# Performance work log

Measured on AMD Instinct MI355X. Metric: run time of the kernel, lower is better.

The kernel has to match this reference:

```python
import jax, jax.numpy as jnp
import numpy as np

N_NODES = 100000
N_EDGES = 1600000
N_GRAPHS = 1024
B = 1024
GNN_INP, GNN_HID, GNN_OUT = 64, 128, 64
INP, HID, OUT = 64, 256, 1
EPS = 1e-5  # torch BatchNorm1d default eps


def _bn(h, gamma, beta):
    # training-mode BatchNorm1d: biased batch statistics over dim 0
    m = h.mean(axis=0)
    v = jnp.mean((h - m) ** 2, axis=0)
    return (h - m) * jax.lax.rsqrt(v + EPS) * gamma + beta


def setup_inputs() -> dict:
    key = jax.random.key(0)
    ks = jax.random.split(key, 24)
    s = 0.05
    inp = {
        "x": jax.random.normal(ks[0], (B, INP), jnp.float32),
        "masks": jax.random.randint(ks[1], (B,), 0, N_GRAPHS),
        "gnn_x": jax.random.normal(ks[2], (N_NODES, GNN_INP), jnp.float32),
        "edge_index": jax.random.randint(ks[3], (2, N_EDGES), 0, N_NODES),
        "gnn_batch": jnp.sort(jax.random.randint(ks[4], (N_NODES,), 0, N_GRAPHS)),
        # GCNConv params
        "W_gcn": jax.random.normal(ks[5], (GNN_INP, GNN_HID), jnp.float32) * s,
        "b_gcn": jnp.zeros((GNN_HID,), jnp.float32),
        "g1": jnp.ones((GNN_HID,), jnp.float32), "be1": jnp.zeros((GNN_HID,), jnp.float32),
        "W_lin1": jax.random.normal(ks[6], (GNN_HID, GNN_HID // 2), jnp.float32) * s,
        "b_lin1": jnp.zeros((GNN_HID // 2,), jnp.float32),
        "g2": jnp.ones((GNN_HID // 2,), jnp.float32), "be2": jnp.zeros((GNN_HID // 2,), jnp.float32),
        "W_lin2": jax.random.normal(ks[7], (GNN_HID // 2, GNN_OUT), jnp.float32) * s,
        "b_lin2": jnp.zeros((GNN_OUT,), jnp.float32),
        "g3": jnp.ones((GNN_OUT,), jnp.float32), "be3": jnp.zeros((GNN_OUT,), jnp.float32),
        # head params
        "W_fc1": jax.random.normal(ks[8], (INP + GNN_OUT, HID), jnp.float32) * s,
        "b_fc1": jnp.zeros((HID,), jnp.float32),
        "g4": jnp.ones((HID,), jnp.float32), "be4": jnp.zeros((HID,), jnp.float32),
        "W_fc2": jax.random.normal(ks[9], (HID, HID // 4), jnp.float32) * s,
        "b_fc2": jnp.zeros((HID // 4,), jnp.float32),
        "g5": jnp.ones((HID // 4,), jnp.float32), "be5": jnp.zeros((HID // 4,), jnp.float32),
        "W_fc3": jax.random.normal(ks[10], (HID // 4, OUT), jnp.float32) * s,
        "b_fc3": jnp.zeros((OUT,), jnp.float32),
    }
    return inp


def _forward(x, masks, gnn_x, edge_index, gnn_batch,
             W_gcn, b_gcn, g1, be1, W_lin1, b_lin1, g2, be2, W_lin2, b_lin2,
             g3, be3, W_fc1, b_fc1, g4, be4, W_fc2, b_fc2, g5, be5, W_fc3, b_fc3):
    N = gnn_x.shape[0]
    # --- GCNConv: linear transform, self-loops, sym-normalized scatter-add ---
    h = gnn_x @ W_gcn  # [N, GNN_HID]
    loop = jnp.arange(N)
    src = jnp.concatenate([edge_index[0], loop])
    dst = jnp.concatenate([edge_index[1], loop])
    deg = jax.ops.segment_sum(jnp.ones_like(dst, jnp.float32), dst, num_segments=N)
    dis = jax.lax.rsqrt(deg)  # deg >= 1 thanks to self-loops
    norm = dis[src] * dis[dst]  # [E+N]
    agg = jax.ops.segment_sum(h[src] * norm[:, None], dst, num_segments=N) + b_gcn
    z = jax.nn.relu(_bn(agg, g1, be1))  # dropout = identity (eval)
    # --- global_mean_pool over graph ids ---
    sums = jax.ops.segment_sum(z, gnn_batch, num_segments=N_GRAPHS)
    cnt = jax.ops.segment_sum(jnp.ones((N,), jnp.float32), gnn_batch, num_segments=N_GRAPHS)
    pooled = sums / jnp.maximum(cnt, 1.0)[:, None]  # [G, GNN_HID]
    z = jax.nn.relu(_bn(pooled @ W_lin1 + b_lin1, g2, be2))
    z = _bn(z @ W_lin2 + b_lin2, g3, be3)  # [G, GNN_OUT]
    # --- MixGNN head ---
    g = z[masks]  # [B, GNN_OUT]
    t = jnp.concatenate([x, g], axis=1)
    t = jax.nn.relu(_bn(t @ W_fc1 + b_fc1, g4, be4))
    t = t * t  # Multiply([h, h])
    t = jax.nn.relu(_bn(t @ W_fc2 + b_fc2, g5, be5))
    t = t * t
    t = t * t
    return t @ W_fc3 + b_fc3  # [B, OUT]


def reference(x, masks, gnn_x, edge_index, gnn_batch,
              W_gcn, b_gcn, g1, be1, W_lin1, b_lin1, g2, be2, W_lin2, b_lin2,
              g3, be3, W_fc1, b_fc1, g4, be4, W_fc2, b_fc2, g5, be5, W_fc3, b_fc3):
    return _forward(x, masks, gnn_x, edge_index, gnn_batch,
                    W_gcn, b_gcn, g1, be1, W_lin1, b_lin1, g2, be2, W_lin2, b_lin2,
                    g3, be3, W_fc1, b_fc1, g4, be4, W_fc2, b_fc2, g5, be5, W_fc3, b_fc3)
```

## Files before the change

### kernel.cpp

```cpp
#include <hip/hip_runtime.h>
#include <hip/hip_bf16.h>

#define N_NODES 100000
#define N_EDGES 1600000
#define N_GRAPHS 1024
#define BSZ 1024
#define EPS 1e-5f

#define NBUCK 256
#define BUCKW 391
#define BCAP  8192
#define SRC_MASK 0x1FFFF
#define BIN_CHUNK 4096
#define BIN_BLOCKS 391
#define NCHUNK 512
#define CHUNK_ROWS 196

#define WS_PSUM    0
#define WS_STATS1  131072
#define WS_STATS2  131200
#define WS_STATS4  131328
#define WS_STATS5  131840
#define WS_M       131968
#define WS_CS      136064
#define WS_ZTOTAL  136128
#define WS_GCUR    136128
#define WS_SCALE1  136384
#define WS_SHIFTP  136512
#define WS_GSTART  136640
#define WS_DIS     137668
#define WS_ROWPTR  237668
#define WS_ROWLEN  337668
#define WS_PACKED  437668
#define WS_CSRC    2534820
#define WS_XH      4631972
#define WS_AGGX    7831972
#define WS_T1      14231972
#define WS_T2      14297508
#define WS_T4      14363044
#define WS_T5      14625188

__device__ inline unsigned short f2bf(float f) {
    unsigned int u = __float_as_uint(f);
    return (unsigned short)((u + 0x7FFFu + ((u >> 16) & 1u)) >> 16);
}

__global__ __launch_bounds__(256) void prep_kernel(float* __restrict__ ws,
                                                   const int* __restrict__ gbatch) {
    int b = blockIdx.x, tid = threadIdx.x;
    if (b < 16) {
        for (int i = b * 256 + tid; i < WS_ZTOTAL; i += 16 * 256) ws[i] = 0.0f;
    } else if (b == 16) {
        ((int*)(ws + WS_GCUR))[tid] = tid * BCAP;
    } else {
        int g = (b - 17) * 256 + tid;
        int lo = 0, hi = N_NODES;
        while (lo < hi) {
            int mid = (lo + hi) >> 1;
            if (gbatch[mid] < g) lo = mid + 1; else hi = mid;
        }
        int* gstart = (int*)(ws + WS_GSTART);
        gstart[g] = lo;
        if (g == 0) gstart[N_GRAPHS] = N_NODES;
    }
}

__global__ __launch_bounds__(256) void cvt_kernel(const float* __restrict__ x,
                                                  unsigned short* __restrict__ xh) {
    int i = blockIdx.x * 256 + threadIdx.x;
    float4 f = ((const float4*)x)[i];
    ushort4 h;
    h.x = f2bf(f.x); h.y = f2bf(f.y); h.z = f2bf(f.z); h.w = f2bf(f.w);
    ((ushort4*)xh)[i] = h;
}

__global__ __launch_bounds__(512) void bin_kernel(const int* __restrict__ ei,
                                                  int* __restrict__ gcursor,
                                                  unsigned int* __restrict__ packed) {
    __shared__ unsigned int stage[BIN_CHUNK];
    __shared__ int lh[NBUCK], lbase[NBUCK], lcur[NBUCK], gb[NBUCK];
    const int* src = ei;
    const int* dst = ei + N_EDGES;
    int tid = threadIdx.x;
    int base = blockIdx.x * BIN_CHUNK;
    int n = min(BIN_CHUNK, N_EDGES - base);
    if (tid < NBUCK) lh[tid] = 0;
    __syncthreads();
    for (int i = tid; i < n; i += 512)
        atomicAdd(&lh[dst[base + i] / BUCKW], 1);
    __syncthreads();
    if (tid < NBUCK) lbase[tid] = lh[tid];
    __syncthreads();
    for (int off = 1; off < NBUCK; off <<= 1) {
        int t = (tid < NBUCK && tid >= off) ? lbase[tid - off] : 0;
        __syncthreads();
        if (tid < NBUCK) lbase[tid] += t;
        __syncthreads();
    }
    if (tid < NBUCK) {
        int excl = lbase[tid] - lh[tid];
        lbase[tid] = excl;
        lcur[tid] = excl;
        gb[tid] = atomicAdd(&gcursor[tid], lh[tid]);
    }
    __syncthreads();
    for (int i = tid; i < n; i += 512) {
        int d = dst[base + i];
        int s = src[base + i];
        int bk = d / BUCKW;
        int dl = d - bk * BUCKW;
        int slot = atomicAdd(&lcur[bk], 1);
        stage[slot] = ((unsigned int)dl << 17) | (unsigned int)s;
    }
    __syncthreads();
    int wid = tid >> 6, lane = tid & 63;
    for (int bk = wid; bk < NBUCK; bk += 8) {
        int lo = lbase[bk], go = gb[bk];
        int len = min(lh[bk], (bk + 1) * BCAP - go);
        for (int j = lane; j < len; j += 64)
            packed[go + j] = stage[lo + j];
    }
}

__global__ __launch_bounds__(512) void csr_build_kernel(const unsigned int* __restrict__ packed,
                                                        const int* __restrict__ gcur,
                                                        int* __restrict__ rowptr,
                                                        int* __restrict__ rowlen,
                                                        int* __restrict__ csrc,
                                                        float* __restrict__ dis) {
    __shared__ int dcnt[BUCKW];
    __shared__ int lcur[BUCKW];
    __shared__ int stage[BCAP];
    int b = blockIdx.x, tid = threadIdx.x;
    int e0 = b * BCAP;
    int ecnt = min(gcur[b] - e0, BCAP);
    int nbase = b * BUCKW;
    int nmax = min(BUCKW, N_NODES - nbase);
    for (int i = tid; i < BUCKW; i += 512) dcnt[i] = 0;
    __syncthreads();
    for (int i = tid; i < ecnt; i += 512)
        atomicAdd(&dcnt[packed[e0 + i] >> 17], 1);
    __syncthreads();
    for (int i = tid; i < nmax; i += 512) {
        dis[nbase + i] = rsqrtf((float)dcnt[i] + 1.0f);
        rowlen[nbase + i] = dcnt[i];
    }
    __syncthreads();
    if (tid < 64) {
        int lane = tid;
        int run = 0;
        for (int c = 0; c < BUCKW; c += 64) {
            int idx = c + lane;
            int v = (idx < BUCKW) ? dcnt[idx] : 0;
            int inc = v;
#pragma unroll
            for (int off = 1; off < 64; off <<= 1) {
                int t = __shfl_up(inc, off);
                if (lane >= off) inc += t;
            }
            if (idx < BUCKW) {
                int excl = run + inc - v;
                dcnt[idx] = excl;
                lcur[idx] = excl;
            }
            run += __shfl(inc, 63);
        }
    }
    __syncthreads();
    for (int i = tid; i < nmax; i += 512)
        rowptr[nbase + i] = e0 + dcnt[i];
    for (int i = tid; i < ecnt; i += 512) {
        unsigned int r = packed[e0 + i];
        int slot = atomicAdd(&lcur[r >> 17], 1);
        stage[slot] = (int)(r & SRC_MASK);
    }
    __syncthreads();
    for (int i = tid; i < ecnt; i += 512) csrc[e0 + i] = stage[i];
}

__global__ __launch_bounds__(256) void gather_kernel(const unsigned short* __restrict__ xh,
                                                     const int* __restrict__ rowptr,
                                                     const int* __restrict__ rowlen,
                                                     const int* __restrict__ csrc,
                                                     const float* __restrict__ dis,
                                                     float* __restrict__ aggx) {
    int wid = (blockIdx.x * 256 + threadIdx.x) >> 6;
    int lane = threadIdx.x & 63;
    if (wid >= N_NODES) return;
    int start = rowptr[wid];
    int len = rowlen[wid];
    float dd = dis[wid];
    float self = __uint_as_float((unsigned int)xh[(size_t)wid * 64 + lane] << 16);
    float acc = self * dd * dd;
    for (int j0 = 0; j0 < len; j0 += 64) {
        int cnt = min(64, len - j0);
        int sv = 0;
        float wv = 0.f;
        if (lane < cnt) {
            sv = csrc[start + j0 + lane];
            wv = dis[sv] * dd;
        }
        int iters = (cnt + 7) & ~7;
        for (int k = 0; k < iters; k += 8) {
            int s[8]; float w[8], v[8];
#pragma unroll
            for (int u = 0; u < 8; ++u) {
                s[u] = __shfl(sv, k + u);
                w[u] = __shfl(wv, k + u);
            }
#pragma unroll
            for (int u = 0; u < 8; ++u)
                v[u] = __uint_as_float((unsigned int)xh[(size_t)s[u] * 64 + lane] << 16);
#pragma unroll
            for (int u = 0; u < 8; ++u) acc = fmaf(v[u], w[u], acc);
        }
    }
    aggx[(size_t)wid * 64 + lane] = acc;
}

__global__ __launch_bounds__(256) void moment_kernel(const float* __restrict__ aggx,
                                                     float* __restrict__ M,
                                                     float* __restrict__ CS) {
    __shared__ float rows[8 * 64];
    int c = blockIdx.x, tid = threadIdx.x;
    int r0 = c * CHUNK_ROWS;
    int r1 = min(r0 + CHUNK_ROWS, N_NODES);
    int i0 = (tid >> 6) * 16;
    int j = tid & 63;
    float acc[16] = {};
    float cs = 0.f;
    for (int it = 0; it < (CHUNK_ROWS + 7) / 8; ++it) {
        int sid = tid * 2;
        int grow = r0 + it * 8 + (sid >> 6);
        float2 v = {0.f, 0.f};
        if (grow < r1) v = *(const float2*)(aggx + (size_t)(r0 + it * 8) * 64 + sid);
        __syncthreads();
        *(float2*)(rows + sid) = v;
        __syncthreads();
#pragma unroll
        for (int rr = 0; rr < 8; ++rr) {
            float bj = rows[rr * 64 + j];
            float4 a0 = *(const float4*)(rows + rr * 64 + i0);
            float4 a1 = *(const float4*)(rows + rr * 64 + i0 + 4);
            float4 a2 = *(const float4*)(rows + rr * 64 + i0 + 8);
            float4 a3 = *(const float4*)(rows + rr * 64 + i0 + 12);
            acc[0]  += a0.x * bj; acc[1]  += a0.y * bj; acc[2]  += a0.z * bj; acc[3]  += a0.w * bj;
            acc[4]  += a1.x * bj; acc[5]  += a1.y * bj; acc[6]  += a1.z * bj; acc[7]  += a1.w * bj;
            acc[8]  += a2.x * bj; acc[9]  += a2.y * bj; acc[10] += a2.z * bj; acc[11] += a2.w * bj;
            acc[12] += a3.x * bj; acc[13] += a3.y * bj; acc[14] += a3.z * bj; acc[15] += a3.w * bj;
        }
        if (tid < 64) {
#pragma unroll
            for (int rr = 0; rr < 8; ++rr) cs += rows[rr * 64 + tid];
        }
    }
#pragma unroll
    for (int m = 0; m < 16; ++m)
        unsafeAtomicAdd(&M[(i0 + m) * 64 + j], acc[m]);
    if (tid < 64) unsafeAtomicAdd(&CS[tid], cs);
}

__global__ __launch_bounds__(64) void fold_kernel(const float* __restrict__ M,
                                                  const float* __restrict__ CS,
                                                  const float* __restrict__ W,
                                                  const float* __restrict__ g1,
                                                  const float* __restrict__ be1,
                                                  float* __restrict__ scale1,
                                                  float* __restrict__ shiftp) {
    __shared__ float wcol[64];
    int j = blockIdx.x;
    int lane = threadIdx.x;
    wcol[lane] = W[lane * 128 + j];
    __syncthreads();
    float wl = wcol[lane];
    float t = 0.f;
    const float* Mrow = M + lane * 64;
#pragma unroll 16
    for (int k = 0; k < 64; ++k) t += Mrow[k] * wcol[k];
    float part = t * wl;
    float csp = CS[lane] * wl;
#pragma unroll
    for (int off = 32; off; off >>= 1) {
        part += __shfl_xor(part, off);
        csp  += __shfl_xor(csp, off);
    }
    if (lane == 0) {
        float Ey2 = part * (1.0f / N_NODES);
        float my = csp * (1.0f / N_NODES);
        float var = Ey2 - my * my;
        float sc = g1[j] * rsqrtf(var + EPS);
        scale1[j] = sc;
        shiftp[j] = be1[j] - my * sc;
    }
}

__global__ __launch_bounds__(256) void gemm_pool_kernel(const float* __restrict__ aggx,
                                                        const int* __restrict__ gbatch,
                                                        const float* __restrict__ W,
                                                        const float* __restrict__ scale1,
                                                        const float* __restrict__ shiftp,
                                                        float* __restrict__ psum) {
    __shared__ float Ws[64 * 128];
    __shared__ float As[16 * 64];
    __shared__ float Zs[16 * 128];
    __shared__ int gid[16];
    int tid = threadIdx.x;
    const float4* W4 = (const float4*)W;
    float4* Ws4 = (float4*)Ws;
#pragma unroll
    for (int i = 0; i < 8; ++i) Ws4[tid + i * 256] = W4[tid + i * 256];
    int row0 = blockIdx.x * 16;
    ((float4*)As)[tid] = ((const float4*)(aggx + (size_t)row0 * 64))[tid];
    if (tid < 16) gid[tid] = gbatch[row0 + tid];
    __syncthreads();
    int tx = tid & 31;
    int ty = tid >> 5;
    int r0 = ty * 2;
    float4 sc4 = ((const float4*)scale1)[tx];
    float4 sh4 = ((const float4*)shiftp)[tx];
    float acc[2][4] = {};
#pragma unroll
    for (int k = 0; k < 64; ++k) {
        float a0 = As[r0 * 64 + k];
        float a1 = As[(r0 + 1) * 64 + k];
        float4 w = Ws4[k * 32 + tx];
        acc[0][0] += a0 * w.x; acc[0][1] += a0 * w.y; acc[0][2] += a0 * w.z; acc[0][3] += a0 * w.w;
        acc[1][0] += a1 * w.x; acc[1][1] += a1 * w.y; acc[1][2] += a1 * w.z; acc[1][3] += a1 * w.w;
    }
#pragma unroll
    for (int rr = 0; rr < 2; ++rr) {
        float4 z;
        z.x = fmaxf(acc[rr][0] * sc4.x + sh4.x, 0.f);
        z.y = fmaxf(acc[rr][1] * sc4.y + sh4.y, 0.f);
        z.z = fmaxf(acc[rr][2] * sc4.z + sh4.z, 0.f);
        z.w = fmaxf(acc[rr][3] * sc4.w + sh4.w, 0.f);
        ((float4*)(Zs + (r0 + rr) * 128))[tx] = z;
    }
    __syncthreads();
    if (tid < 128) {
        int c = tid;
        float a = 0.f;
        int g = gid[0];
#pragma unroll
        for (int i = 0; i < 16; ++i) {
            int gi = gid[i];
            if (gi != g) {
                unsafeAtomicAdd(&psum[(size_t)g * 128 + c], a);
                a = 0.f;
                g = gi;
            }
            a += Zs[i * 128 + c];
        }
        unsafeAtomicAdd(&psum[(size_t)g * 128 + c], a);
    }
}

__global__ __launch_bounds__(256) void lin1_kernel(const float* __restrict__ psum,
                                                   const int* __restrict__ gstart,
                                                   const float* __restrict__ W,
                                                   const float* __restrict__ bias,
                                                   float* __restrict__ t1,
                                                   float* __restrict__ stats1) {
    __shared__ float ls[256], ls2[256];
    int tid = threadIdx.x;
    int r = blockIdx.x * 4 + (tid >> 6);
    int c = tid & 63;
    float invc = 1.0f / fmaxf((float)(gstart[r + 1] - gstart[r]), 1.0f);
    float acc = 0.f;
    const float* srow = psum + (size_t)r * 128;
#pragma unroll 8
    for (int k = 0; k < 128; ++k)
        acc += srow[k] * W[k * 64 + c];
    acc = bias[c] + acc * invc;
    t1[r * 64 + c] = acc;
    ls[tid] = acc; ls2[tid] = acc * acc;
    __syncthreads();
    if (tid < 64) {
        float s = ls[tid] + ls[tid + 64] + ls[tid + 128] + ls[tid + 192];
        float q = ls2[tid] + ls2[tid + 64] + ls2[tid + 128] + ls2[tid + 192];
        unsafeAtomicAdd(&stats1[c], s);
        unsafeAtomicAdd(&stats1[64 + c], q);
    }
}

__global__ __launch_bounds__(256) void lin2_kernel(const float* __restrict__ t1,
                                                   const float* __restrict__ stats1,
                                                   const float* __restrict__ g,
                                                   const float* __restrict__ be,
                                                   const float* __restrict__ W,
                                                   const float* __restrict__ bias,
                                                   float* __restrict__ t2,
                                                   float* __restrict__ stats2) {
    __shared__ float sc[64], sh[64];
    __shared__ float ls[256], ls2[256];
    int tid = threadIdx.x;
    if (tid < 64) {
        float m = stats1[tid] * (1.0f / BSZ);
        float var = stats1[64 + tid] * (1.0f / BSZ) - m * m;
        float s = g[tid] * rsqrtf(var + EPS);
        sc[tid] = s; sh[tid] = be[tid] - m * s;
    }
    __syncthreads();
    int r = blockIdx.x * 4 + (tid >> 6);
    int c = tid & 63;
    float acc = bias[c];
    const float* row = t1 + (size_t)r * 64;
#pragma unroll 8
    for (int k = 0; k < 64; ++k) {
        float z = fmaxf(row[k] * sc[k] + sh[k], 0.f);
        acc += z * W[k * 64 + c];
    }
    t2[r * 64 + c] = acc;
    ls[tid] = acc; ls2[tid] = acc * acc;
    __syncthreads();
    if (tid < 64) {
        float s = ls[tid] + ls[tid + 64] + ls[tid + 128] + ls[tid + 192];
        float q = ls2[tid] + ls2[tid + 64] + ls2[tid + 128] + ls2[tid + 192];
        unsafeAtomicAdd(&stats2[c], s);
        unsafeAtomicAdd(&stats2[64 + c], q);
    }
}

__global__ __launch_bounds__(1024) void fc1_kernel(const float* __restrict__ x,
                                                   const int* __restrict__ masks,
                                                   const float* __restrict__ t2,
                                                   const float* __restrict__ stats2,
                                                   const float* __restrict__ g3,
                                                   const float* __restrict__ be3,
                                                   const float* __restrict__ W,
                                                   const float* __restrict__ bias,
                                                   float* __restrict__ t4,
                                                   float* __restrict__ stats4) {
    __shared__ float sc[64], sh[64];
    __shared__ float cat[4][128];
    __shared__ float ls[1024], ls2[1024];
    int tid = threadIdx.x;
    if (tid < 64) {
        float m = stats2[tid] * (1.0f / BSZ);
        float var = stats2[64 + tid] * (1.0f / BSZ) - m * m;
        float s = g3[tid] * rsqrtf(var + EPS);
        sc[tid] = s; sh[tid] = be3[tid] - m * s;
    }
    __syncthreads();
    int r0 = blockIdx.x * 4;
    if (tid < 512) {
        int i = tid >> 7;
        int k = tid & 127;
        int r = r0 + i;
        float v;
        if (k < 64) {
            v = x[r * 64 + k];
        } else {
            int mrow = masks[r];
            int kk = k - 64;
            v = t2[mrow * 64 + kk] * sc[kk] + sh[kk];
        }
        cat[i][k] = v;
    }
    __syncthreads();
    int i = tid >> 8;
    int c = tid & 255;
    float acc = bias[c];
#pragma unroll 8
    for (int k = 0; k < 128; ++k)
        acc += cat[i][k] * W[k * 256 + c];
    t4[(size_t)(r0 + i) * 256 + c] = acc;
    ls[tid] = acc; ls2[tid] = acc * acc;
    __syncthreads();
    if (tid < 256) {
        float s = ls[tid] + ls[tid + 256] + ls[tid + 512] + ls[tid + 768];
        float q = ls2[tid] + ls2[tid + 256] + ls2[tid + 512] + ls2[tid + 768];
        unsafeAtomicAdd(&stats4[c], s);
        unsafeAtomicAdd(&stats4[256 + c], q);
    }
}

__global__ __launch_bounds__(256) void fc2_kernel(const float* __restrict__ t4,
                                                  const float* __restrict__ stats4,
                                                  const float* __restrict__ g4,
                                                  const float* __restrict__ be4,
                                                  const float* __restrict__ W,
                                                  const float* __restrict__ bias,
                                                  float* __restrict__ t5,
                                                  float* __restrict__ stats5) {
    __shared__ float sc[256], sh[256];
    __shared__ float ls[256], ls2[256];
    int tid = threadIdx.x;
    {
        float m = stats4[tid] * (1.0f / BSZ);
        float var = stats4[256 + tid] * (1.0f / BSZ) - m * m;
        float s = g4[tid] * rsqrtf(var + EPS);
        sc[tid] = s; sh[tid] = be4[tid] - m * s;
    }
    __syncthreads();
    int r = blockIdx.x * 4 + (tid >> 6);
    int c = tid & 63;
    float acc = bias[c];
    const float* row = t4 + (size_t)r * 256;
#pragma unroll 8
    for (int k = 0; k < 256; ++k) {
        float z = fmaxf(row[k] * sc[k] + sh[k], 0.f);
        z *= z;
        acc += z * W[k * 64 + c];
    }
    t5[r * 64 + c] = acc;
    ls[tid] = acc; ls2[tid] = acc * acc;
    __syncthreads();
    if (tid < 64) {
        float s = ls[tid] + ls[tid + 64] + ls[tid + 128] + ls[tid + 192];
        float q = ls2[tid] + ls2[tid + 64] + ls2[tid + 128] + ls2[tid + 192];
        unsafeAtomicAdd(&stats5[c], s);
        unsafeAtomicAdd(&stats5[64 + c], q);
    }
}

__global__ __launch_bounds__(256) void fc3_kernel(const float* __restrict__ t5,
                                                  const float* __restrict__ stats5,
                                                  const float* __restrict__ g5,
                                                  const float* __restrict__ be5,
                                                  const float* __restrict__ W,
                                                  const float* __restrict__ bias,
                                                  float* __restrict__ out) {
    __shared__ float sc[64], sh[64];
    int tid = threadIdx.x;
    if (tid < 64) {
        float m = stats5[tid] * (1.0f / BSZ);
        float var = stats5[64 + tid] * (1.0f / BSZ) - m * m;
        float s = g5[tid] * rsqrtf(var + EPS);
        sc[tid] = s; sh[tid] = be5[tid] - m * s;
    }
    __syncthreads();
    int r = blockIdx.x * 256 + tid;
    float acc = bias[0];
    const float* row = t5 + (size_t)r * 64;
#pragma unroll
    for (int k = 0; k < 64; ++k) {
        float z = fmaxf(row[k] * sc[k] + sh[k], 0.f);
        z = z * z;
        z = z * z;
        acc += z * W[k];
    }
    out[r] = acc;
}

extern "C" void kernel_launch(void* const* d_in, const int* in_sizes, int n_in,
                              void* d_out, int out_size, void* d_ws, size_t ws_size,
                              hipStream_t stream) {
    const float* x      = (const float*)d_in[0];
    const int*   masks  = (const int*)d_in[1];
    const float* gnn_x  = (const float*)d_in[2];
    const int*   ei     = (const int*)d_in[3];
    const int*   gbatch = (const int*)d_in[4];
    const float* W_gcn  = (const float*)d_in[5];
    const float* b_gcn  = (const float*)d_in[6];
    const float* g1     = (const float*)d_in[7];
    const float* be1    = (const float*)d_in[8];
    const float* W_lin1 = (const float*)d_in[9];
    const float* b_lin1 = (const float*)d_in[10];
    const float* g2     = (const float*)d_in[11];
    const float* be2    = (const float*)d_in[12];
    const float* W_lin2 = (const float*)d_in[13];
    const float* b_lin2 = (const float*)d_in[14];
    const float* g3     = (const float*)d_in[15];
    const float* be3    = (const float*)d_in[16];
    const float* W_fc1  = (const float*)d_in[17];
    const float* b_fc1  = (const float*)d_in[18];
    const float* g4     = (const float*)d_in[19];
    const float* be4    = (const float*)d_in[20];
    const float* W_fc2  = (const float*)d_in[21];
    const float* b_fc2  = (const float*)d_in[22];
    const float* g5     = (const float*)d_in[23];
    const float* be5    = (const float*)d_in[24];
    const float* W_fc3  = (const float*)d_in[25];
    const float* b_fc3  = (const float*)d_in[26];
    (void)b_gcn;

    float* ws = (float*)d_ws;
    float* psum   = ws + WS_PSUM;
    float* stats1 = ws + WS_STATS1;
    float* stats2 = ws + WS_STATS2;
    float* stats4 = ws + WS_STATS4;
    float* stats5 = ws + WS_STATS5;
    float* Mbuf   = ws + WS_M;
    float* CSbuf  = ws + WS_CS;
    int*   gcur   = (int*)(ws + WS_GCUR);
    float* scale1 = ws + WS_SCALE1;
    float* shiftp = ws + WS_SHIFTP;
    int*   gstart = (int*)(ws + WS_GSTART);
    float* dis    = ws + WS_DIS;
    int*   rowptr = (int*)(ws + WS_ROWPTR);
    int*   rowlen = (int*)(ws + WS_ROWLEN);
    unsigned int* packed = (unsigned int*)(ws + WS_PACKED);
    int*   csrc   = (int*)(ws + WS_CSRC);
    unsigned short* xh = (unsigned short*)(ws + WS_XH);
    float* aggx   = ws + WS_AGGX;
    float* t1     = ws + WS_T1;
    float* t2     = ws + WS_T2;
    float* t4     = ws + WS_T4;
    float* t5     = ws + WS_T5;
    float* out    = (float*)d_out;

    prep_kernel<<<21, 256, 0, stream>>>(ws, gbatch);
    cvt_kernel<<<N_NODES * 64 / 4 / 256, 256, 0, stream>>>(gnn_x, xh);
    bin_kernel<<<BIN_BLOCKS, 512, 0, stream>>>(ei, gcur, packed);
    csr_build_kernel<<<NBUCK, 512, 0, stream>>>(packed, gcur, rowptr, rowlen, csrc, dis);
    gather_kernel<<<(N_NODES * 64 + 255) / 256, 256, 0, stream>>>(xh, rowptr, rowlen, csrc, dis, aggx);
    moment_kernel<<<NCHUNK, 256, 0, stream>>>(aggx, Mbuf, CSbuf);
    fold_kernel<<<128, 64, 0, stream>>>(Mbuf, CSbuf, W_gcn, g1, be1, scale1, shiftp);
    gemm_pool_kernel<<<N_NODES / 16, 256, 0, stream>>>(aggx, gbatch, W_gcn, scale1, shiftp, psum);
    lin1_kernel<<<256, 256, 0, stream>>>(psum, gstart, W_lin1, b_lin1, t1, stats1);
    lin2_kernel<<<256, 256, 0, stream>>>(t1, stats1, g2, be2, W_lin2, b_lin2, t2, stats2);
    fc1_kernel<<<256, 1024, 0, stream>>>(x, masks, t2, stats2, g3, be3, W_fc1, b_fc1, t4, stats4);
    fc2_kernel<<<256, 256, 0, stream>>>(t4, stats4, g4, be4, W_fc2, b_fc2, t5, stats5);
    fc3_kernel<<<4, 256, 0, stream>>>(t5, stats5, g5, be5, W_fc3, b_fc3, out);
}
```

Baseline: 244.3 us.

## Replace CSR build with windowed LDS-atomic scatter aggregation over dst buckets

Drops the per-bucket CSR construction (row pointers, prefix scan, source reorder) and instead aggregates neighbor features straight from the bucketed packed edge list. Each block owns a window of destination nodes and accumulates into shared memory with atomics. A lighter kernel now computes only degrees. The cvt and prep kernels are merged to save a launch. The catch is that every block rescans its whole bucket, 4x redundant reads of the packed edges, and shared-memory float atomics replace register accumulation.

```diff
diff --git a/kernel.cpp b/kernel.cpp
--- a/kernel.cpp
+++ b/kernel.cpp
@@ -15,6 +15,9 @@
 #define BIN_BLOCKS 391
 #define NCHUNK 512
 #define CHUNK_ROWS 196
+#define WINW 98
+#define NWIN 4
+#define CVT_BLOCKS 6250
 
 #define WS_PSUM    0
 #define WS_STATS1  131072
@@ -29,31 +32,36 @@
 #define WS_SHIFTP  136512
 #define WS_GSTART  136640
 #define WS_DIS     137668
-#define WS_ROWPTR  237668
-#define WS_ROWLEN  337668
-#define WS_PACKED  437668
-#define WS_CSRC    2534820
-#define WS_XH      4631972
-#define WS_AGGX    7831972
-#define WS_T1      14231972
-#define WS_T2      14297508
-#define WS_T4      14363044
-#define WS_T5      14625188
+#define WS_PACKED  237668
+#define WS_XH      2334820
+#define WS_AGGX    5534820
+#define WS_T1      11934820
+#define WS_T2      12000356
+#define WS_T4      12065892
+#define WS_T5      12328036
 
 __device__ inline unsigned short f2bf(float f) {
     unsigned int u = __float_as_uint(f);
     return (unsigned short)((u + 0x7FFFu + ((u >> 16) & 1u)) >> 16);
 }
 
-__global__ __launch_bounds__(256) void prep_kernel(float* __restrict__ ws,
-                                                   const int* __restrict__ gbatch) {
+__global__ __launch_bounds__(256) void prep_cvt_kernel(float* __restrict__ ws,
+                                                       const int* __restrict__ gbatch,
+                                                       const float* __restrict__ x,
+                                                       unsigned short* __restrict__ xh) {
     int b = blockIdx.x, tid = threadIdx.x;
-    if (b < 16) {
-        for (int i = b * 256 + tid; i < WS_ZTOTAL; i += 16 * 256) ws[i] = 0.0f;
-    } else if (b == 16) {
+    if (b < CVT_BLOCKS) {
+        int i = b * 256 + tid;
+        float4 f = ((const float4*)x)[i];
+        ushort4 h;
+        h.x = f2bf(f.x); h.y = f2bf(f.y); h.z = f2bf(f.z); h.w = f2bf(f.w);
+        ((ushort4*)xh)[i] = h;
+    } else if (b < CVT_BLOCKS + 16) {
+        for (int i = (b - CVT_BLOCKS) * 256 + tid; i < WS_ZTOTAL; i += 16 * 256) ws[i] = 0.0f;
+    } else if (b == CVT_BLOCKS + 16) {
         ((int*)(ws + WS_GCUR))[tid] = tid * BCAP;
     } else {
-        int g = (b - 17) * 256 + tid;
+        int g = (b - (CVT_BLOCKS + 17)) * 256 + tid;
         int lo = 0, hi = N_NODES;
         while (lo < hi) {
             int mid = (lo + hi) >> 1;
@@ -65,15 +73,6 @@
     }
 }
 
-__global__ __launch_bounds__(256) void cvt_kernel(const float* __restrict__ x,
-                                                  unsigned short* __restrict__ xh) {
-    int i = blockIdx.x * 256 + threadIdx.x;
-    float4 f = ((const float4*)x)[i];
-    ushort4 h;
-    h.x = f2bf(f.x); h.y = f2bf(f.y); h.z = f2bf(f.z); h.w = f2bf(f.w);
-    ((ushort4*)xh)[i] = h;
-}
-
 __global__ __launch_bounds__(512) void bin_kernel(const int* __restrict__ ei,
                                                   int* __restrict__ gcursor,
                                                   unsigned int* __restrict__ packed) {
@@ -122,100 +121,71 @@
     }
 }
 
-__global__ __launch_bounds__(512) void csr_build_kernel(const unsigned int* __restrict__ packed,
-                                                        const int* __restrict__ gcur,
-                                                        int* __restrict__ rowptr,
-                                                        int* __restrict__ rowlen,
-                                                        int* __restrict__ csrc,
-                                                        float* __restrict__ dis) {
+__global__ __launch_bounds__(256) void degdis_kernel(const unsigned int* __restrict__ packed,
+                                                     const int* __restrict__ gcur,
+                                                     float* __restrict__ dis) {
     __shared__ int dcnt[BUCKW];
-    __shared__ int lcur[BUCKW];
-    __shared__ int stage[BCAP];
     int b = blockIdx.x, tid = threadIdx.x;
     int e0 = b * BCAP;
     int ecnt = min(gcur[b] - e0, BCAP);
     int nbase = b * BUCKW;
     int nmax = min(BUCKW, N_NODES - nbase);
-    for (int i = tid; i < BUCKW; i += 512) dcnt[i] = 0;
-    __syncthreads();
-    for (int i = tid; i < ecnt; i += 512)
+    for (int i = tid; i < BUCKW; i += 256) dcnt[i] = 0;
+    __syncthreads();
+    for (int i = tid; i < ecnt; i += 256)
         atomicAdd(&dcnt[packed[e0 + i] >> 17], 1);
     __syncthreads();
-    for (int i = tid; i < nmax; i += 512) {
+    for (int i = tid; i < nmax; i += 256)
         dis[nbase + i] = rsqrtf((float)dcnt[i] + 1.0f);
-        rowlen[nbase + i] = dcnt[i];
-    }
-    __syncthreads();
-    if (tid < 64) {
-        int lane = tid;
-        int run = 0;
-        for (int c = 0; c < BUCKW; c += 64) {
-            int idx = c + lane;
-            int v = (idx < BUCKW) ? dcnt[idx] : 0;
-            int inc = v;
-#pragma unroll
-            for (int off = 1; off < 64; off <<= 1) {
-                int t = __shfl_up(inc, off);
-                if (lane >= off) inc += t;
-            }
-            if (idx < BUCKW) {
-                int excl = run + inc - v;
-                dcnt[idx] = excl;
-                lcur[idx] = excl;
-            }
-            run += __shfl(inc, 63);
-        }
-    }
-    __syncthreads();
-    for (int i = tid; i < nmax; i += 512)
-        rowptr[nbase + i] = e0 + dcnt[i];
-    for (int i = tid; i < ecnt; i += 512) {
-        unsigned int r = packed[e0 + i];
-        int slot = atomicAdd(&lcur[r >> 17], 1);
-        stage[slot] = (int)(r & SRC_MASK);
-    }
-    __syncthreads();
-    for (int i = tid; i < ecnt; i += 512) csrc[e0 + i] = stage[i];
-}
-
-__global__ __launch_bounds__(256) void gather_kernel(const unsigned short* __restrict__ xh,
-                                                     const int* __restrict__ rowptr,
-                                                     const int* __restrict__ rowlen,
-                                                     const int* __restrict__ csrc,
+}
+
+__global__ __launch_bounds__(512) void gather_kernel(const unsigned short* __restrict__ xh,
+                                                     const unsigned int* __restrict__ packed,
+                                                     const int* __restrict__ gcur,
                                                      const float* __restrict__ dis,
                                                      float* __restrict__ aggx) {
-    int wid = (blockIdx.x * 256 + threadIdx.x) >> 6;
-    int lane = threadIdx.x & 63;
-    if (wid >= N_NODES) return;
-    int start = rowptr[wid];
-    int len = rowlen[wid];
-    float dd = dis[wid];
-    float self = __uint_as_float((unsigned int)xh[(size_t)wid * 64 + lane] << 16);
-    float acc = self * dd * dd;
-    for (int j0 = 0; j0 < len; j0 += 64) {
-        int cnt = min(64, len - j0);
-        int sv = 0;
-        float wv = 0.f;
-        if (lane < cnt) {
-            sv = csrc[start + j0 + lane];
-            wv = dis[sv] * dd;
+    __shared__ float acc[WINW * 64];
+    __shared__ float disw[WINW];
+    int blk = blockIdx.x;
+    int b = blk >> 2;
+    int w = blk & 3;
+    int wlo = w * WINW;
+    int nbase = b * BUCKW + wlo;
+    int nwin = min(WINW, min(BUCKW - wlo, N_NODES - nbase));
+    if (nwin <= 0) return;
+    int tid = threadIdx.x;
+    int lane = tid & 63, wave = tid >> 6;
+    for (int i = tid; i < WINW * 64; i += 512) acc[i] = 0.f;
+    if (tid < nwin) disw[tid] = dis[nbase + tid];
+    __syncthreads();
+    int e0 = b * BCAP;
+    int ecnt = min(gcur[b] - e0, BCAP);
+    int whi = wlo + nwin;
+    for (int c0 = wave * 64; c0 < ecnt; c0 += 512) {
+        int n = min(64, ecnt - c0);
+        unsigned int rec = (lane < n) ? packed[e0 + c0 + lane] : 0xFFFFFFFFu;
+        int dl = (int)(rec >> 17);
+        bool m = (dl >= wlo) && (dl < whi);
+        float wv = m ? dis[rec & SRC_MASK] : 0.f;
+        unsigned long long mask = __ballot(m);
+        while (mask) {
+            int p = __ffsll(mask) - 1;
+            mask &= mask - 1;
+            unsigned int r = __shfl(rec, p);
+            float ws = __shfl(wv, p);
+            int dloc = (int)(r >> 17) - wlo;
+            int s = (int)(r & SRC_MASK);
+            float v = __uint_as_float((unsigned int)xh[(size_t)s * 64 + lane] << 16);
+            atomicAdd(&acc[dloc * 64 + lane], v * (ws * disw[dloc]));
         }
-        int iters = (cnt + 7) & ~7;
-        for (int k = 0; k < iters; k += 8) {
-            int s[8]; float w[8], v[8];
-#pragma unroll
-            for (int u = 0; u < 8; ++u) {
-                s[u] = __shfl(sv, k + u);
-                w[u] = __shfl(wv, k + u);
-            }
-#pragma unroll
-            for (int u = 0; u < 8; ++u)
-                v[u] = __uint_as_float((unsigned int)xh[(size_t)s[u] * 64 + lane] << 16);
-#pragma unroll
-            for (int u = 0; u < 8; ++u) acc = fmaf(v[u], w[u], acc);
-        }
-    }
-    aggx[(size_t)wid * 64 + lane] = acc;
+    }
+    __syncthreads();
+    for (int nl = wave; nl < nwin; nl += 8) {
+        int node = nbase + nl;
+        float dd = disw[nl];
+        float self = __uint_as_float((unsigned int)xh[(size_t)node * 64 + lane] << 16);
+        aggx[(size_t)node * 64 + lane] = acc[nl * 64 + lane] + self * dd * dd;
+    }
 }
 
 __global__ __launch_bounds__(256) void moment_kernel(const float* __restrict__ aggx,
@@ -588,10 +558,7 @@
     float* shiftp = ws + WS_SHIFTP;
     int*   gstart = (int*)(ws + WS_GSTART);
     float* dis    = ws + WS_DIS;
-    int*   rowptr = (int*)(ws + WS_ROWPTR);
-    int*   rowlen = (int*)(ws + WS_ROWLEN);
     unsigned int* packed = (unsigned int*)(ws + WS_PACKED);
-    int*   csrc   = (int*)(ws + WS_CSRC);
     unsigned short* xh = (unsigned short*)(ws + WS_XH);
     float* aggx   = ws + WS_AGGX;
     float* t1     = ws + WS_T1;
@@ -600,11 +567,10 @@
     float* t5     = ws + WS_T5;
     float* out    = (float*)d_out;
 
-    prep_kernel<<<21, 256, 0, stream>>>(ws, gbatch);
-    cvt_kernel<<<N_NODES * 64 / 4 / 256, 256, 0, stream>>>(gnn_x, xh);
+    prep_cvt_kernel<<<CVT_BLOCKS + 21, 256, 0, stream>>>(ws, gbatch, gnn_x, xh);
     bin_kernel<<<BIN_BLOCKS, 512, 0, stream>>>(ei, gcur, packed);
-    csr_build_kernel<<<NBUCK, 512, 0, stream>>>(packed, gcur, rowptr, rowlen, csrc, dis);
-    gather_kernel<<<(N_NODES * 64 + 255) / 256, 256, 0, stream>>>(xh, rowptr, rowlen, csrc, dis, aggx);
+    degdis_kernel<<<NBUCK, 256, 0, stream>>>(packed, gcur, dis);
+    gather_kernel<<<NBUCK * NWIN, 512, 0, stream>>>(xh, packed, gcur, dis, aggx);
     moment_kernel<<<NCHUNK, 256, 0, stream>>>(aggx, Mbuf, CSbuf);
     fold_kernel<<<128, 64, 0, stream>>>(Mbuf, CSbuf, W_gcn, g1, be1, scale1, shiftp);
     gemm_pool_kernel<<<N_NODES / 16, 256, 0, stream>>>(aggx, gbatch, W_gcn, scale1, shiftp, psum);
```

Result: slower. 760.2 us (+211.1%).
